# Kernel tuning notes

Measured on AMD Instinct MI355X. Metric: run time of the kernel, lower is better.

## Reference

```python
import jax, jax.numpy as jnp
import numpy as np

B = 2048        # patients (segments)
K = 4           # images per patient
C = 1280        # backbone_out (tf_efficientnet_b0)
PAIRS = K * (K - 1) // 2  # torch.combinations -> 6
NCLS = 1
N_DROP = 5


def setup_inputs() -> dict:
    key = jax.random.key(0)
    ks = jax.random.split(key, 8)
    x = jax.random.normal(ks[0], (B * K, C), jnp.float32)  # detached backbone features
    ids2 = jnp.repeat(jnp.arange(B, dtype=jnp.int32), PAIRS)  # segment id per pair
    Wc = jax.random.normal(ks[1], (C, C, 2), jnp.float32) * 0.02  # Conv1d(C,C,k=2) weight
    bc = jnp.zeros((C,), jnp.float32)
    W0 = jax.random.normal(ks[2], (NCLS, C), jnp.float32) * 0.02
    b0 = jnp.zeros((NCLS,), jnp.float32)
    W1 = jax.random.normal(ks[3], (1, C), jnp.float32) * 0.02
    b1 = jnp.zeros((1,), jnp.float32)
    W2 = jax.random.normal(ks[4], (1, C), jnp.float32) * 0.02
    b2 = jnp.zeros((1,), jnp.float32)
    return dict(x=x, ids2=ids2, Wc=Wc, bc=bc, W0=W0, b0=b0, W1=W1, b1=b1, W2=W2, b2=b2)


def reference(x, ids2, Wc, bc, W0, b0, W1, b1, W2, b2):
    # --- pair combinations within each patient group of K images ---
    ii, jj = np.triu_indices(K, 1)               # static [PAIRS]
    xg = x.reshape(B, K, C)
    xa = xg[:, ii].reshape(B * PAIRS, C)         # first element of each pair
    xb = xg[:, jj].reshape(B * PAIRS, C)         # second element
    # Conv1d(C, C, kernel=2) over the length-2 pair sequence + ReLU
    xc = jax.nn.relu(xa @ Wc[:, :, 0].T + xb @ Wc[:, :, 1].T + bc)  # [P, C]

    # --- 5 fixed dropout masks (p=0.5, train-mode scaling) ---
    masks = jax.random.bernoulli(jax.random.key(42), 0.5,
                                 (N_DROP, xc.shape[0], C)).astype(xc.dtype) * 2.0
    xd = xc[None] * masks                        # [D, P, C]

    cnt = jax.ops.segment_sum(jnp.ones_like(ids2, dtype=xc.dtype),
                              ids2, num_segments=B)  # [B], == PAIRS

    def agg(W, b):
        # head -> scalar mean over classes -> segment-mean over pairs -> mean over dropouts
        z = (jnp.einsum('dpc,oc->dpo', xd, W) + b).mean(-1)          # [D, P]
        s = jax.vmap(lambda u: jax.ops.segment_sum(u, ids2, num_segments=B))(z)
        return (s / cnt).mean(0)                                      # [B]

    logits = agg(W0, b0)
    logits1 = agg(W1, b1)
    logits2 = agg(W2, b2)
    return jnp.stack([logits, logits1, logits2], axis=1)  # [B, 3]
```

## Files before the change

kernel.cpp:

```cpp
#include <hip/hip_runtime.h>


typedef __attribute__((ext_vector_type(8))) short short8;
typedef __attribute__((ext_vector_type(4))) float f32x4;

#define PLANE 15728640u
#define KS2   (0x1BD11BDAu ^ 42u)

__device__ __forceinline__ unsigned short f2bf(float f) {
  unsigned int u = __builtin_bit_cast(unsigned int, f);
  u = (u + 0x7FFFu + ((u >> 16) & 1u)) >> 16;
  return (unsigned short)u;
}
__device__ __forceinline__ float bf2f(unsigned short h) {
  unsigned int u = ((unsigned int)h) << 16;
  return __builtin_bit_cast(float, u);
}

__global__ __launch_bounds__(256) void prep(
    const float* __restrict__ x, unsigned short* __restrict__ xb,
    const float* __restrict__ Wc, unsigned short* __restrict__ Wb) {
  const int bid = blockIdx.x;
  const int t = threadIdx.x;
  if (bid < 2560) {
#pragma unroll
    for (int p = 0; p < 4; p++) {
      const int i4 = bid * 1024 + p * 256 + t;
      const float4 v = ((const float4*)x)[i4];
      ushort4 o;
      o.x = f2bf(v.x); o.y = f2bf(v.y); o.z = f2bf(v.z); o.w = f2bf(v.w);
      ((ushort4*)xb)[i4] = o;
    }
  } else {
    const int i = (bid - 2560) * 256 + t;
    const int n = i / 640;
    const int cin = (i - n * 640) * 2;
    const float4 v = *(const float4*)(Wc + n * 2560 + cin * 2);
    *(ushort2*)(Wb + n * 2560 + cin) =
        make_ushort2(f2bf(v.x), f2bf(v.z));
    *(ushort2*)(Wb + n * 2560 + 1280 + cin) =
        make_ushort2(f2bf(v.y), f2bf(v.w));
  }
}

#define GL_LDS(g, l) __builtin_amdgcn_global_load_lds( \
    (const __attribute__((address_space(1))) unsigned int*)(g), \
    (__attribute__((address_space(3))) unsigned int*)(l), 16, 0, 0)

__global__ __launch_bounds__(256) void gemm_u(
    const unsigned short* __restrict__ Xb,
    const unsigned short* __restrict__ Wb,
    unsigned short* __restrict__ U0b,
    unsigned short* __restrict__ U1b)
{
  __shared__ unsigned short sA[128 * 32];
  __shared__ unsigned short sB[128 * 32];
  const int t = threadIdx.x;
  const int xcd = blockIdx.x & 7;
  const int slot = blockIdx.x >> 3;
  const int mband = xcd * 8 + slot / 20;
  const int nst = slot % 20;
  const int side = nst / 10;
  const int n0 = (nst % 10) * 128;
  const int p0 = mband * 128;

  const int lane = t & 63, w = t >> 6;
  const int wr = w >> 1, wc = w & 1;
  const int mrow = lane & 15;
  const int koff = (lane >> 4) * 8;
  const int srow = lane >> 2, schk = (lane & 3) * 8;

  unsigned short* const ldsA0 = sA + (w * 32 + 0) * 32;
  unsigned short* const ldsA1 = sA + (w * 32 + 16) * 32;
  unsigned short* const ldsB0 = sB + (w * 32 + 0) * 32;
  unsigned short* const ldsB1 = sB + (w * 32 + 16) * 32;
  const unsigned short* const gA0 = Xb + (p0 + w * 32 + srow) * 1280 + schk;
  const unsigned short* const gA1 = Xb + (p0 + w * 32 + 16 + srow) * 1280 + schk;
  const unsigned short* const gB0 =
      Wb + (n0 + w * 32 + srow) * 2560 + side * 1280 + schk;
  const unsigned short* const gB1 =
      Wb + (n0 + w * 32 + 16 + srow) * 2560 + side * 1280 + schk;

  f32x4 acc[4][4];
#pragma unroll
  for (int i = 0; i < 4; i++)
#pragma unroll
    for (int j = 0; j < 4; j++) acc[i][j] = (f32x4){0.f, 0.f, 0.f, 0.f};

  for (int k0 = 0; k0 < 1280; k0 += 32) {
    __syncthreads();
    GL_LDS(gA0 + k0, ldsA0);
    GL_LDS(gA1 + k0, ldsA1);
    GL_LDS(gB0 + k0, ldsB0);
    GL_LDS(gB1 + k0, ldsB1);
    __syncthreads();
    short8 af[4], bfr[4];
#pragma unroll
    for (int i = 0; i < 4; i++)
      af[i] = *(const short8*)(sA + (wr * 64 + i * 16 + mrow) * 32 + koff);
#pragma unroll
    for (int j = 0; j < 4; j++)
      bfr[j] = *(const short8*)(sB + (wc * 64 + j * 16 + mrow) * 32 + koff);
#pragma unroll
    for (int i = 0; i < 4; i++)
#pragma unroll
      for (int j = 0; j < 4; j++)
        acc[i][j] = __builtin_amdgcn_mfma_f32_16x16x32_bf16(af[i], bfr[j],
                                                            acc[i][j], 0, 0, 0);
  }

  unsigned short* const U = side ? U1b : U0b;
  const int mq = (lane >> 4) * 4;
  const int nn = lane & 15;
#pragma unroll
  for (int j = 0; j < 4; j++) {
    const int n = n0 + wc * 64 + j * 16 + nn;
#pragma unroll
    for (int i = 0; i < 4; i++) {
      const int prow = p0 + wr * 64 + i * 16 + mq;
#pragma unroll
      for (int rg = 0; rg < 4; rg++)
        U[(prow + rg) * 1280 + n] = f2bf(acc[i][j][rg]);
    }
  }
}

__device__ __forceinline__ unsigned int rotl(unsigned int x, int r) {
  return __builtin_amdgcn_alignbit(x, x, 32 - r);
}
__device__ __forceinline__ unsigned int tf_msb(unsigned int c) {
  unsigned int x0 = c;
  unsigned int x1 = rotl(c, 13) ^ c;
  x0 += x1; x1 = rotl(x1, 15) ^ x0;
  x0 += x1; x1 = rotl(x1, 26) ^ x0;
  x0 += x1; x1 = rotl(x1, 6)  ^ x0;
  unsigned int t;
  t = x1 + (KS2 + 1u); x0 = x0 + t + 42u; x1 = rotl(t, 17) ^ x0;
  x0 += x1; x1 = rotl(x1, 29) ^ x0;
  x0 += x1; x1 = rotl(x1, 16) ^ x0;
  x0 += x1; x1 = rotl(x1, 24) ^ x0;
  t = x1 + 2u; x0 = x0 + t + KS2; x1 = rotl(t, 13) ^ x0;
  x0 += x1; x1 = rotl(x1, 15) ^ x0;
  x0 += x1; x1 = rotl(x1, 26) ^ x0;
  x0 += x1; x1 = rotl(x1, 6)  ^ x0;
  t = x1 + 45u; x0 = x0 + t; x1 = rotl(t, 17) ^ x0;
  x0 += x1; x1 = rotl(x1, 29) ^ x0;
  x0 += x1; x1 = rotl(x1, 16) ^ x0;
  x0 += x1; x1 = rotl(x1, 24) ^ x0;
  t = x1 + (KS2 + 4u); x0 = x0 + t + 42u; x1 = rotl(t, 13) ^ x0;
  x0 += x1; x1 = rotl(x1, 15) ^ x0;
  x0 += x1; x1 = rotl(x1, 26) ^ x0;
  x0 += x1; x1 = rotl(x1, 6)  ^ x0;
  return ((x0 + KS2) ^ (x1 + 5u)) >> 31;
}

__global__ __launch_bounds__(256) void rng_pk(unsigned int* __restrict__ Spk) {
  const int t = threadIdx.x;
  const int D0 = blockIdx.x * 1024 + t;
  for (int g = 0; g < 4; ++g) {
    const int D = D0 + g * 256;
    const unsigned int bg = (unsigned int)D * 8u + 42u;
    unsigned int zacc = 0;
#pragma unroll
    for (int sub = 0; sub < 8; ++sub) {
      const unsigned int b = bg + (unsigned int)sub;
      const unsigned int z5 = tf_msb(b) + tf_msb(b + PLANE) +
                              tf_msb(b + 2u * PLANE) + tf_msb(b + 3u * PLANE) +
                              tf_msb(b + 4u * PLANE);
      zacc |= z5 << (4 * sub);
    }
    Spk[D] = zacc;
  }
}

__global__ __launch_bounds__(256) void combine(
    const unsigned short* __restrict__ U0b, const unsigned short* __restrict__ U1b,
    const unsigned int* __restrict__ Spk, const float* __restrict__ bc,
    const float* __restrict__ W0, const float* __restrict__ W1,
    const float* __restrict__ W2,
    const float* __restrict__ b0, const float* __restrict__ b1,
    const float* __restrict__ b2, float* __restrict__ out)
{
  const int pat = blockIdx.x;
  const int t = threadIdx.x;
  const int rbase = pat * 4 * 1280;
  const int sbase = pat * 6 * 160;
  float s0 = 0.f, s1 = 0.f, s2 = 0.f;

  for (int qi = 0; qi < 5; qi++) {
    const int c = qi * 256 + t;
    const float w0 = W0[c], w1 = W1[c], w2 = W2[c], bcv = bc[c];
    const float u00 = bf2f(U0b[rbase + c]);
    const float u01 = bf2f(U0b[rbase + 1280 + c]);
    const float u02 = bf2f(U0b[rbase + 2560 + c]);
    const float u11 = bf2f(U1b[rbase + 1280 + c]);
    const float u12 = bf2f(U1b[rbase + 2560 + c]);
    const float u13 = bf2f(U1b[rbase + 3840 + c]);
    const float pv[6] = {u00 + u11, u00 + u12, u00 + u13,
                         u01 + u12, u01 + u13, u02 + u13};
    const int cd = c >> 3, cn = 4 * (c & 7);
#pragma unroll
    for (int pr = 0; pr < 6; pr++) {
      float v = pv[pr] + bcv;
      v = v > 0.f ? v : 0.f;
      const int z = (int)((Spk[sbase + pr * 160 + cd] >> cn) & 7u);
      const float tx = v * (float)(5 - z);
      s0 += tx * w0; s1 += tx * w1; s2 += tx * w2;
    }
  }

#pragma unroll
  for (int off = 32; off > 0; off >>= 1) {
    s0 += __shfl_xor(s0, off); s1 += __shfl_xor(s1, off); s2 += __shfl_xor(s2, off);
  }
  __shared__ float red[4][3];
  const int lane = t & 63, w = t >> 6;
  if (lane == 0) { red[w][0] = s0; red[w][1] = s1; red[w][2] = s2; }
  __syncthreads();
  if (t == 0) {
    const float r0 = red[0][0] + red[1][0] + red[2][0] + red[3][0];
    const float r1 = red[0][1] + red[1][1] + red[2][1] + red[3][1];
    const float r2 = red[0][2] + red[1][2] + red[2][2] + red[3][2];
    out[pat * 3 + 0] = b0[0] + r0 * (1.0f / 15.0f);
    out[pat * 3 + 1] = b1[0] + r1 * (1.0f / 15.0f);
    out[pat * 3 + 2] = b2[0] + r2 * (1.0f / 15.0f);
  }
}

extern "C" void kernel_launch(void* const* d_in, const int* in_sizes, int n_in,
                              void* d_out, int out_size, void* d_ws, size_t ws_size,
                              hipStream_t stream) {
  const float* x  = (const float*)d_in[0];
  const float* Wc = (const float*)d_in[2];
  const float* bc = (const float*)d_in[3];
  const float* W0 = (const float*)d_in[4];
  const float* b0 = (const float*)d_in[5];
  const float* W1 = (const float*)d_in[6];
  const float* b1 = (const float*)d_in[7];
  const float* W2 = (const float*)d_in[8];
  const float* b2 = (const float*)d_in[9];
  float* out = (float*)d_out;

  char* ws = (char*)d_ws;
  unsigned short* xb  = (unsigned short*)ws;
  unsigned short* Wb  = (unsigned short*)(ws + 20971520);
  unsigned short* U0b = (unsigned short*)(ws + 27525120);
  unsigned short* U1b = (unsigned short*)(ws + 48496640);
  unsigned int*   Spk = (unsigned int*)(ws + 69468160);

  prep<<<5760, 256, 0, stream>>>(x, xb, Wc, Wb);
  gemm_u<<<1280, 256, 0, stream>>>(xb, Wb, U0b, U1b);
  rng_pk<<<1920, 256, 0, stream>>>(Spk);
  combine<<<2048, 256, 0, stream>>>(U0b, U1b, Spk, bc, W0, W1, W2,
                                    b0, b1, b2, out);
}
```

Baseline: 318.4 us.

## Fuse dropout RNG generation into combine kernel, split patients across two blocks

Removes the separate rng_pk kernel and the packed mask buffer: the Threefry dropout bits are now generated inline in the combine kernel, which is split into two blocks per patient (three pairs each). Output is pre-initialised with biases in the prep kernel, and each half-block atomically adds its partial sum. This saves a launch and the global round-trip of the mask words but recomputes RNG where it's consumed, and it adds atomics whose summation order is nondeterministic.

Result: faster. 310.7 us (-2.4%).

```diff
diff --git a/kernel.cpp b/kernel.cpp
--- a/kernel.cpp
+++ b/kernel.cpp
@@ -19,7 +19,9 @@
 
 __global__ __launch_bounds__(256) void prep(
     const float* __restrict__ x, unsigned short* __restrict__ xb,
-    const float* __restrict__ Wc, unsigned short* __restrict__ Wb) {
+    const float* __restrict__ Wc, unsigned short* __restrict__ Wb,
+    const float* __restrict__ b0, const float* __restrict__ b1,
+    const float* __restrict__ b2, float* __restrict__ out) {
   const int bid = blockIdx.x;
   const int t = threadIdx.x;
   if (bid < 2560) {
@@ -31,7 +33,7 @@
       o.x = f2bf(v.x); o.y = f2bf(v.y); o.z = f2bf(v.z); o.w = f2bf(v.w);
       ((ushort4*)xb)[i4] = o;
     }
-  } else {
+  } else if (bid < 5760) {
     const int i = (bid - 2560) * 256 + t;
     const int n = i / 640;
     const int cin = (i - n * 640) * 2;
@@ -40,6 +42,12 @@
         make_ushort2(f2bf(v.x), f2bf(v.z));
     *(ushort2*)(Wb + n * 2560 + 1280 + cin) =
         make_ushort2(f2bf(v.y), f2bf(v.w));
+  } else {
+    const int i = (bid - 5760) * 256 + t;
+    if (i < 2048 * 3) {
+      const int h = i % 3;
+      out[i] = (h == 0) ? b0[0] : ((h == 1) ? b1[0] : b2[0]);
+    }
   }
 }
 
@@ -154,57 +162,45 @@
   return ((x0 + KS2) ^ (x1 + 5u)) >> 31;
 }
 
-__global__ __launch_bounds__(256) void rng_pk(unsigned int* __restrict__ Spk) {
+__global__ __launch_bounds__(256) void rng_combine(
+    const unsigned short* __restrict__ U0b, const unsigned short* __restrict__ U1b,
+    const float* __restrict__ bc,
+    const float* __restrict__ W0, const float* __restrict__ W1,
+    const float* __restrict__ W2, float* __restrict__ out)
+{
+  const int b = blockIdx.x;
+  const int pat = b >> 1, trip = b & 1;
   const int t = threadIdx.x;
-  const int D0 = blockIdx.x * 1024 + t;
-  for (int g = 0; g < 4; ++g) {
-    const int D = D0 + g * 256;
-    const unsigned int bg = (unsigned int)D * 8u + 42u;
-    unsigned int zacc = 0;
-#pragma unroll
-    for (int sub = 0; sub < 8; ++sub) {
-      const unsigned int b = bg + (unsigned int)sub;
-      const unsigned int z5 = tf_msb(b) + tf_msb(b + PLANE) +
-                              tf_msb(b + 2u * PLANE) + tf_msb(b + 3u * PLANE) +
-                              tf_msb(b + 4u * PLANE);
-      zacc |= z5 << (4 * sub);
-    }
-    Spk[D] = zacc;
-  }
-}
-
-__global__ __launch_bounds__(256) void combine(
-    const unsigned short* __restrict__ U0b, const unsigned short* __restrict__ U1b,
-    const unsigned int* __restrict__ Spk, const float* __restrict__ bc,
-    const float* __restrict__ W0, const float* __restrict__ W1,
-    const float* __restrict__ W2,
-    const float* __restrict__ b0, const float* __restrict__ b1,
-    const float* __restrict__ b2, float* __restrict__ out)
-{
-  const int pat = blockIdx.x;
-  const int t = threadIdx.x;
-  const int rbase = pat * 4 * 1280;
-  const int sbase = pat * 6 * 160;
+  const int rbase = pat * 5120;
   float s0 = 0.f, s1 = 0.f, s2 = 0.f;
 
   for (int qi = 0; qi < 5; qi++) {
     const int c = qi * 256 + t;
     const float w0 = W0[c], w1 = W1[c], w2 = W2[c], bcv = bc[c];
-    const float u00 = bf2f(U0b[rbase + c]);
-    const float u01 = bf2f(U0b[rbase + 1280 + c]);
-    const float u02 = bf2f(U0b[rbase + 2560 + c]);
-    const float u11 = bf2f(U1b[rbase + 1280 + c]);
-    const float u12 = bf2f(U1b[rbase + 2560 + c]);
-    const float u13 = bf2f(U1b[rbase + 3840 + c]);
-    const float pv[6] = {u00 + u11, u00 + u12, u00 + u13,
-                         u01 + u12, u01 + u13, u02 + u13};
-    const int cd = c >> 3, cn = 4 * (c & 7);
-#pragma unroll
-    for (int pr = 0; pr < 6; pr++) {
+    float pv[3];
+    if (trip == 0) {
+      const float u00 = bf2f(U0b[rbase + c]);
+      pv[0] = u00 + bf2f(U1b[rbase + 1280 + c]);
+      pv[1] = u00 + bf2f(U1b[rbase + 2560 + c]);
+      pv[2] = u00 + bf2f(U1b[rbase + 3840 + c]);
+    } else {
+      const float u01 = bf2f(U0b[rbase + 1280 + c]);
+      const float u02 = bf2f(U0b[rbase + 2560 + c]);
+      const float u12 = bf2f(U1b[rbase + 2560 + c]);
+      const float u13 = bf2f(U1b[rbase + 3840 + c]);
+      pv[0] = u01 + u12; pv[1] = u01 + u13; pv[2] = u02 + u13;
+    }
+    const unsigned int base =
+        (unsigned int)((pat * 6 + trip * 3) * 1280 + c) + 42u;
+#pragma unroll
+    for (int pr = 0; pr < 3; pr++) {
+      const unsigned int cb = base + (unsigned int)(pr * 1280);
+      const unsigned int z = tf_msb(cb) + tf_msb(cb + PLANE) +
+                             tf_msb(cb + 2u * PLANE) + tf_msb(cb + 3u * PLANE) +
+                             tf_msb(cb + 4u * PLANE);
       float v = pv[pr] + bcv;
       v = v > 0.f ? v : 0.f;
-      const int z = (int)((Spk[sbase + pr * 160 + cd] >> cn) & 7u);
-      const float tx = v * (float)(5 - z);
+      const float tx = v * (float)(5 - (int)z);
       s0 += tx * w0; s1 += tx * w1; s2 += tx * w2;
     }
   }
@@ -217,13 +213,9 @@
   const int lane = t & 63, w = t >> 6;
   if (lane == 0) { red[w][0] = s0; red[w][1] = s1; red[w][2] = s2; }
   __syncthreads();
-  if (t == 0) {
-    const float r0 = red[0][0] + red[1][0] + red[2][0] + red[3][0];
-    const float r1 = red[0][1] + red[1][1] + red[2][1] + red[3][1];
-    const float r2 = red[0][2] + red[1][2] + red[2][2] + red[3][2];
-    out[pat * 3 + 0] = b0[0] + r0 * (1.0f / 15.0f);
-    out[pat * 3 + 1] = b1[0] + r1 * (1.0f / 15.0f);
-    out[pat * 3 + 2] = b2[0] + r2 * (1.0f / 15.0f);
+  if (t < 3) {
+    const float s = red[0][t] + red[1][t] + red[2][t] + red[3][t];
+    atomicAdd(&out[pat * 3 + t], s * (1.0f / 15.0f));
   }
 }
 
@@ -246,11 +238,8 @@
   unsigned short* Wb  = (unsigned short*)(ws + 20971520);
   unsigned short* U0b = (unsigned short*)(ws + 27525120);
   unsigned short* U1b = (unsigned short*)(ws + 48496640);
-  unsigned int*   Spk = (unsigned int*)(ws + 69468160);
-
-  prep<<<5760, 256, 0, stream>>>(x, xb, Wc, Wb);
+
+  prep<<<5784, 256, 0, stream>>>(x, xb, Wc, Wb, b0, b1, b2, out);
   gemm_u<<<1280, 256, 0, stream>>>(xb, Wb, U0b, U1b);
-  rng_pk<<<1920, 256, 0, stream>>>(Spk);
-  combine<<<2048, 256, 0, stream>>>(U0b, U1b, Spk, bc, W0, W1, W2,
-                                    b0, b1, b2, out);
-}
+  rng_combine<<<4096, 256, 0, stream>>>(U0b, U1b, bc, W0, W1, W2, out);
+}
```
